# Kernel optimization log

Hardware: AMD Instinct MI355X
Metric: run time of the kernel (lower is better)

Reference implementation:

```python
import jax, jax.numpy as jnp
import numpy as np

B, TQ, TK, D, R, H = 4, 2048, 2048, 1024, 64, 512
TAU_BASE, ASTRO_DECAY = 1.0, 0.95


def setup_inputs() -> dict:
    key = jax.random.key(0)
    ks = jax.random.split(key, 20)
    xav = lambda k, din, dout: jax.random.uniform(k, (din, dout), jnp.float32, -1.0, 1.0) * np.sqrt(6.0 / (din + dout))
    inp = {
        'q_in': jax.random.normal(ks[0], (B, TQ, D), jnp.float32),
        'k_in': jax.random.normal(ks[1], (B, TK, D), jnp.float32),
        'v_in': jax.random.normal(ks[2], (B, TK, D), jnp.float32),
        'astrocyte_state': jnp.zeros((B,), jnp.float32),
        'Wq': xav(ks[3], D, D), 'bq': jnp.zeros((D,), jnp.float32),
        'Wk': xav(ks[4], D, D), 'bk': jnp.zeros((D,), jnp.float32),
        'Wv': xav(ks[5], D, D), 'bv': jnp.zeros((D,), jnp.float32),
        'Wo': xav(ks[6], D, D), 'bo': jnp.zeros((D,), jnp.float32),
        # orthonormal role rows (R <= D): QR of a random D x R matrix, rows = Q^T
        'role_matrix': jnp.linalg.qr(jax.random.normal(ks[7], (D, R), jnp.float32))[0].T,
        'Wr1': xav(ks[8], D, H), 'br1': jnp.zeros((H,), jnp.float32),
        'Wr2': xav(ks[9], H, R),
        'astro_scale': jnp.ones((1,), jnp.float32),
    }
    return inp


def _l2norm(x, axis=-1, eps=1e-12):
    return x / jnp.clip(jnp.linalg.norm(x, axis=axis, keepdims=True), eps)


def _bind_vectors(a, b):
    # holographic (circular-convolution) binding via FFT along feature dim
    n = a.shape[-1]
    return jnp.fft.irfft(jnp.fft.rfft(a, axis=-1) * jnp.fft.rfft(b, axis=-1), n=n, axis=-1)


def _compute_surprise(Q):
    # per-token surprise: RMS-normalized L2 magnitude of projected queries -> (B, T_q)
    return jnp.linalg.norm(Q, axis=-1) / np.sqrt(Q.shape[-1])


def reference(q_in, k_in, v_in, astrocyte_state, Wq, bq, Wk, bk, Wv, bv, Wo, bo,
              role_matrix, Wr1, br1, Wr2, astro_scale):
    Q = q_in @ Wq + bq                      # (B,TQ,D)
    K = k_in @ Wk + bk                      # (B,TK,D)
    V = v_in @ Wv + bv                      # (B,TK,D)

    role_mat_norm = _l2norm(role_matrix)    # (R,D)
    role_logits = jax.nn.relu(K @ Wr1 + br1) @ Wr2          # (B,TK,R)
    role_weights = jax.nn.softmax(role_logits, axis=-1)
    role_vecs = role_weights @ role_mat_norm                 # (B,TK,D)
    K_bound = _bind_vectors(K, role_vecs)                    # (B,TK,D)

    surprise = _compute_surprise(Q)                          # (B,TQ)
    mean_surprise = surprise.mean(axis=-1)                   # (B,)
    new_state = ASTRO_DECAY * astrocyte_state + (1.0 - ASTRO_DECAY) * mean_surprise
    tau_eff = TAU_BASE * jnp.clip(1.0 + astro_scale * new_state, 0.001)[:, None, None]

    q_n = _l2norm(Q)
    k_n = _l2norm(K_bound)
    cos_sim = jnp.einsum('bqd,bkd->bqk', q_n, k_n)           # (B,TQ,TK)
    x = (cos_sim + 1.0) * 0.5
    scores = jnp.clip(1.0 - tau_eff * (1.0 - x) ** 2, 0.0)   # Epanechnikov kernel
    attn = scores / jnp.clip(scores.sum(axis=-1, keepdims=True), 1e-9)
    context = jnp.einsum('bqk,bkd->bqd', attn, V)
    output = context @ Wo + bo
    return output, new_state
```

## Files before the change

### kernel.cpp

```cpp
#include <hip/hip_runtime.h>
#include <stdint.h>


#define Bq 4
#define Tq 2048
#define Dd 1024
#define NT 8192
#define Hh 512
#define Rr_ 64
#define FQ 1024

typedef unsigned short ushort_t;
typedef short s16x8 __attribute__((ext_vector_type(8)));
typedef float floatx4 __attribute__((ext_vector_type(4)));

__device__ __forceinline__ float b2f(ushort_t s) {
  unsigned u = (unsigned)s << 16;
  return __builtin_bit_cast(float, u);
}
__device__ __forceinline__ ushort_t f2b(float f) {
  unsigned u = __builtin_bit_cast(unsigned, f);
  unsigned r = (u + 0x7fffu + ((u >> 16) & 1u)) >> 16;
  return (ushort_t)r;
}
// ... 88 lines not shown
#pragma unroll
    for (int i = 0; i < 4; i++)
      af[i] = *(const s16x8*)&As[(wm + i * 16 + fr) * 32 + fk];
#pragma unroll
    for (int j = 0; j < 4; j++)
      bfv[j] = *(const s16x8*)&Bs[(wn + j * 16 + fr) * 32 + fk];
#pragma unroll
    for (int i = 0; i < 4; i++)
#pragma unroll
      for (int j = 0; j < 4; j++)
        acc[i][j] = __builtin_amdgcn_mfma_f32_16x16x32_bf16(af[i], bfv[j], acc[i][j], 0, 0, 0);
    __syncthreads();
  }

  const float tv = o.tau ? o.tau[bz] : 0.f;
  float*   Cp  = o.C   ? o.C   + (size_t)bz * o.sC : nullptr;
  ushort_t* Cb = o.Cbf ? o.Cbf + (size_t)bz * o.sC : nullptr;
  float bcv[4], cmv[4];
#pragma unroll
  for (int j = 0; j < 4; j++) {
    const int col = tn + wn + j * 16 + (lane & 15);
    bcv[j] = o.bias_col ? o.bias_col[col] : 0.f;
    cmv[j] = o.cmul ? o.cmul[(size_t)bz * o.cmulStride + col] : 1.f;
  }
#pragma unroll
  for (int i = 0; i < 4; i++) {
#pragma unroll
    for (int r = 0; r < 4; r++) {
      const int row = tm + wm + i * 16 + (lane >> 4) * 4 + r;
      const float rm = o.rmul ? o.rmul[(size_t)bz * o.rmulStride + row] : 1.f;
      const float br = o.bias_row ? o.bias_row[row] : 0.f;
      float rsum = 0.f;
#pragma unroll
      for (int j = 0; j < 4; j++) {
        const int col = tn + wn + j * 16 + (lane & 15);
        float v;
        if (o.flags & 2) {
          v = acc[i][j][r] * (rm * cmv[j]) + bcv[j] + br;
        } else {
          v = (acc[i][j][r] + bcv[j] + br) * (rm * cmv[j]);
        }
        if (o.flags & 1) v = fmaxf(v, 0.f);
        if (o.tau) { float d = 1.0f - v; v = fmaxf(1.0f - tv * 0.25f * d * d, 0.f); }
        rsum += (o.rsMode == 2) ? v * v : v;
        if (Cp) Cp[(size_t)row * o.ldc + col] = v;
        if (Cb) Cb[(size_t)row * o.ldc + col] = f2b(v);
      }
      if (o.rsMode == 1 || o.rsMode == 2) {
        rsum += __shfl_xor(rsum, 1);
        rsum += __shfl_xor(rsum, 2);
        rsum += __shfl_xor(rsum, 4);
        rsum += __shfl_xor(rsum, 8);
        if ((lane & 15) == 0)
// ... 123 lines not shown
    STAGE256(t2, 1, sl);
    __builtin_amdgcn_s_barrier();
    __builtin_amdgcn_s_setprio(1);
#pragma unroll
    for (int m = 0; m < 8; m++)
#pragma unroll
      for (int n = 2; n < 4; n++)
        acc[m][n] = __builtin_amdgcn_mfma_f32_16x16x32_bf16(a[m], b[n], acc[m][n], 0, 0, 0);
    __builtin_amdgcn_s_setprio(0);
    asm volatile("s_waitcnt vmcnt(4)" ::: "memory");
    __builtin_amdgcn_s_barrier();
  }
#undef STAGE256

  const float tv = o.tau ? o.tau[bz] : 0.f;
  float*   Cp  = o.C   ? o.C   + (size_t)bz * o.sC : nullptr;
  ushort_t* Cb = o.Cbf ? o.Cbf + (size_t)bz * o.sC : nullptr;
  float bcv[4], cmv[4];
#pragma unroll
  for (int n = 0; n < 4; n++) {
    const int col = tn + wn * 64 + n * 16 + (lane & 15);
    bcv[n] = o.bias_col ? o.bias_col[col] : 0.f;
    cmv[n] = o.cmul ? o.cmul[(size_t)bz * o.cmulStride + col] : 1.f;
  }
#pragma unroll
  for (int m = 0; m < 8; m++) {
#pragma unroll
    for (int r = 0; r < 4; r++) {
      const int row = tm + wm * 128 + m * 16 + (lane >> 4) * 4 + r;
      const float rm = o.rmul ? o.rmul[(size_t)bz * o.rmulStride + row] : 1.f;
      const float br = o.bias_row ? o.bias_row[row] : 0.f;
      float rsum = 0.f;
#pragma unroll
      for (int n = 0; n < 4; n++) {
        const int col = tn + wn * 64 + n * 16 + (lane & 15);
        float v;
        if (o.flags & 2) {
          v = acc[m][n][r] * (rm * cmv[n]) + bcv[n] + br;
        } else {
          v = (acc[m][n][r] + bcv[n] + br) * (rm * cmv[n]);
        }
        if (o.flags & 1) v = fmaxf(v, 0.f);
        if (o.tau) { float d = 1.0f - v; v = fmaxf(1.0f - tv * 0.25f * d * d, 0.f); }
        rsum += (o.rsMode == 2) ? v * v : v;
        if (Cp) Cp[(size_t)row * o.ldc + col] = v;
        if (Cb) Cb[(size_t)row * o.ldc + col] = f2b(v);
      }
      if (o.rsMode == 1 || o.rsMode == 2) {
        rsum += __shfl_xor(rsum, 1);
        rsum += __shfl_xor(rsum, 2);
        rsum += __shfl_xor(rsum, 4);
        rsum += __shfl_xor(rsum, 8);
        if ((lane & 15) == 0)
// ... 54 lines not shown
#pragma unroll
    for (int i = 0; i < 4; i++)
      af[i] = *(const s16x8*)&As[(wm + i * 16 + fr) * 32 + fk];
#pragma unroll
    for (int j = 0; j < 4; j++)
      bfv[j] = *(const s16x8*)&Bs[(wn + j * 16 + fr) * 32 + fk];
#pragma unroll
    for (int i = 0; i < 4; i++)
#pragma unroll
      for (int j = 0; j < 4; j++)
        acc[i][j] = __builtin_amdgcn_mfma_f32_16x16x32_bf16(af[i], bfv[j], acc[i][j], 0, 0, 0);
    __syncthreads();
  }

  const float tv = tau ? tau[bz] : 0.f;
  float*   Cp  = C   ? C   + (size_t)bz * sC : nullptr;
  ushort_t* Cb = Cbf ? Cbf + (size_t)bz * sC : nullptr;
  float bcv[4], cmv[4];
#pragma unroll
  for (int j = 0; j < 4; j++) {
    const int col = tn + wn + j * 16 + (lane & 15);
    bcv[j] = bias_col ? bias_col[col] : 0.f;
    cmv[j] = cmul ? cmul[(size_t)bz * cmulStride + col] : 1.f;
  }
#pragma unroll
  for (int i = 0; i < 4; i++) {
#pragma unroll
    for (int r = 0; r < 4; r++) {
      const int row = tm + wm + i * 16 + (lane >> 4) * 4 + r;
      const float rm = rmul ? rmul[(size_t)bz * rmulStride + row] : 1.f;
      const float br = bias_row ? bias_row[row] : 0.f;
      float rsum = 0.f;
#pragma unroll
      for (int j = 0; j < 4; j++) {
        const int col = tn + wn + j * 16 + (lane & 15);
        float v;
        if (flags & 2) {
          v = acc[i][j][r] * (rm * cmv[j]) + bcv[j] + br;
        } else {
          v = (acc[i][j][r] + bcv[j] + br) * (rm * cmv[j]);
        }
        if (flags & 1) v = fmaxf(v, 0.f);
        if (tau) { float d = 1.0f - v; v = fmaxf(1.0f - tv * 0.25f * d * d, 0.f); }
        rsum += (rsMode == 2) ? v * v : v;
        if (Cp) Cp[(size_t)row * ldc + col] = v;
        if (Cb) Cb[(size_t)row * ldc + col] = f2b(v);
      }
      if (rsMode == 1 || rsMode == 2) {
        rsum += __shfl_xor(rsum, 1);
        rsum += __shfl_xor(rsum, 2);
        rsum += __shfl_xor(rsum, 4);
        rsum += __shfl_xor(rsum, 8);
        if ((lane & 15) == 0)
          atomicAdd(&rowsum[(size_t)bz * rsStride + row], rsum);
      }
    }
  }
}

struct P3 { const ushort_t* A[3]; const ushort_t* Bt[3]; ushort_t* C[3]; int M[3]; };

__global__ __launch_bounds__(256) void prep3(P3 p) {
  __shared__ __align__(16) ushort_t As[128 * 32];
  __shared__ __align__(16) ushort_t Bs[128 * 32];
  const int z  = blockIdx.z;
  const int tm = blockIdx.y * 128;
  if (tm >= p.M[z]) return;
  const ushort_t* Ab = p.A[z];
  const ushort_t* Bb = p.Bt[z];
  ushort_t*       Cc = p.C[z];
  const int tn   = blockIdx.x * 128;
  const int tid  = threadIdx.x;
  const int wave = tid >> 6;
  const int lane = tid & 63;
  const int wm   = (wave & 1) << 6;
  const int wn   = (wave >> 1) << 6;
  const int sr   = lane >> 2;
  const int cp   = lane & 3;
  const int sc   = (((cp - (sr >> 1)) & 3) << 3);
  const int fr   = lane & 15;
  const int fk   = ((((lane >> 4) + (fr >> 1)) & 3) << 3);

  floatx4 acc[4][4] = {};

  for (int k0 = 0; k0 < Dd; k0 += 32) {
    {
      const ushort_t* gA0 = Ab + (size_t)(tm + wave * 16 + sr) * Dd + (k0 + sc);
      const ushort_t* gA1 = gA0 + (size_t)64 * Dd;
      char* lA = (char*)As + wave * 1024;
      load_lds16(gA0, lA);
      load_lds16(gA1, lA + 4096);
      const ushort_t* gB0 = Bb + (size_t)(tn + wave * 16 + sr) * Dd + (k0 + sc);
      const ushort_t* gB1 = gB0 + (size_t)64 * Dd;
      char* lB = (char*)Bs + wave * 1024;
      load_lds16(gB0, lB);
      load_lds16(gB1, lB + 4096);
    }
    __syncthreads();
    s16x8 af[4], bfv[4];
#pragma unroll
    for (int i = 0; i < 4; i++)
      af[i] = *(const s16x8*)&As[(wm + i * 16 + fr) * 32 + fk];
#pragma unroll
    for (int j = 0; j < 4; j++)
      bfv[j] = *(const s16x8*)&Bs[(wn + j * 16 + fr) * 32 + fk];
#pragma unroll
    for (int i = 0; i < 4; i++)
#pragma unroll
      for (int j = 0; j < 4; j++)
        acc[i][j] = __builtin_amdgcn_mfma_f32_16x16x32_bf16(af[i], bfv[j], acc[i][j], 0, 0, 0);
    __syncthreads();
  }

#pragma unroll
  for (int i = 0; i < 4; i++)
#pragma unroll
    for (int r = 0; r < 4; r++) {
      const int row = tm + wm + i * 16 + (lane >> 4) * 4 + r;
#pragma unroll
      for (int j = 0; j < 4; j++) {
        const int col = tn + wn + j * 16 + (lane & 15);
        Cc[(size_t)row * Dd + col] = f2b(acc[i][j][r]);
      }
    }
}

__global__ __launch_bounds__(256) void castbf(const float* __restrict__ in,
                                              ushort_t* __restrict__ out, int n4) {
  int i = blockIdx.x * 256 + threadIdx.x;
  if (i >= n4) return;
  float4 v = ((const float4*)in)[i];
  ushort4 o;
  o.x = f2b(v.x); o.y = f2b(v.y); o.z = f2b(v.z); o.w = f2b(v.w);
  ((ushort4*)out)[i] = o;
}

struct C3 { const float* in[3]; ushort_t* out[3]; };
__global__ __launch_bounds__(256) void castbf3(C3 p) {
  int z = blockIdx.y;
  int i = blockIdx.x * 256 + threadIdx.x;
  float4 v = ((const float4*)p.in[z])[i];
  ushort4 o;
  o.x = f2b(v.x); o.y = f2b(v.y); o.z = f2b(v.z); o.w = f2b(v.w);
  ((ushort4*)p.out[z])[i] = o;
}

struct TC4 { const float* in[4]; ushort_t* out[4]; };
__global__ __launch_bounds__(256) void tcast4(TC4 p) {
  __shared__ float t[32][33];
  int z = blockIdx.z;
  const float* in = p.in[z];
  ushort_t* out = p.out[z];
  int r0 = blockIdx.x * 32, c0 = blockIdx.y * 32;
  int x = threadIdx.x, y = threadIdx.y;
  for (int dy = 0; dy < 32; dy += 8)
    t[y + dy][x] = in[(size_t)(r0 + y + dy) * 1024 + c0 + x];
  __syncthreads();
  for (int dy = 0; dy < 32; dy += 8)
    out[(size_t)(c0 + y + dy) * 1024 + r0 + x] = f2b(t[x][y + dy]);
}

__global__ __launch_bounds__(256) void tcast(const float* __restrict__ in,
                                             ushort_t* __restrict__ out,
                                             int RrN, int Cc, int Cp) {
  __shared__ float t[32][33];
  int r0 = blockIdx.x * 32, c0 = blockIdx.y * 32;
  int x = threadIdx.x, y = threadIdx.y;
  for (int dy = 0; dy < 32; dy += 8) {
    int r = r0 + y + dy, c = c0 + x;
    t[y + dy][x] = (c < Cc) ? in[(size_t)r * Cc + c] : 0.f;
  }
  __syncthreads();
  for (int dy = 0; dy < 32; dy += 8) {
    int c = c0 + y + dy, r = r0 + x;
    if (c < Cp) out[(size_t)c * RrN + r] = f2b(t[x][y + dy]);
  }
}

__global__ __launch_bounds__(256) void rolenorm(const float* __restrict__ rm,
                                                ushort_t* __restrict__ rmn) {
  int r = blockIdx.x, tid = threadIdx.x;
  float4 v = ((const float4*)(rm + (size_t)r * 1024))[tid];
  float s = v.x * v.x + v.y * v.y + v.z * v.z + v.w * v.w;
#pragma unroll
  for (int m = 1; m < 64; m <<= 1) s += __shfl_xor(s, m);
  __shared__ float red[6];
  if ((tid & 63) == 0) red[tid >> 6] = s;
  __syncthreads();
  if (tid == 0) red[4] = 1.f / fmaxf(sqrtf(red[0] + red[1] + red[2] + red[3]), 1e-12f);
  __syncthreads();
  float inv = red[4];
  ushort4 o;
  o.x = f2b(v.x * inv); o.y = f2b(v.y * inv); o.z = f2b(v.z * inv); o.w = f2b(v.w * inv);
  ((ushort4*)(rmn + (size_t)r * 1024))[tid] = o;
}

__global__ __launch_bounds__(256) void rfn_kernel(const ushort_t* __restrict__ rmn,
                                                  const ushort_t* __restrict__ ftab,
                                                  ushort_t* __restrict__ RFnT) {
  int f = blockIdx.x;
  int t = threadIdx.x;
  int r = t >> 2, part = t & 3;
  const ushort_t* fr = ftab + (size_t)f * 1024 + part * 256;
  const ushort_t* rr = rmn + (size_t)r * 1024 + part * 256;
  float s = 0.f;
#pragma unroll 4
  for (int i = 0; i < 32; i++) {
    s16x8 a = *(const s16x8*)(fr + i * 8);
    s16x8 b = *(const s16x8*)(rr + i * 8);
#pragma unroll
    for (int j = 0; j < 8; j++) s += b2f((ushort_t)a[j]) * b2f((ushort_t)b[j]);
  }
  s += __shfl_xor(s, 1);
  s += __shfl_xor(s, 2);
  if (part == 0) RFnT[(size_t)f * 128 + r] = f2b(s);
}

__global__ __launch_bounds__(64) void foldbk(const ushort_t* __restrict__ ftab,
                                             const float* __restrict__ bk,
                                             float* __restrict__ bkF) {
  int j = blockIdx.x, lane = threadIdx.x;
  const ushort_t* row = ftab + (size_t)j * 1024 + lane * 16;
  const float* bp = bk + lane * 16;
  float s = 0.f;
#pragma unroll
  for (int i = 0; i < 2; i++) {
    s16x8 a = *(const s16x8*)(row + i * 8);
#pragma unroll
    for (int e = 0; e < 8; e++) s += b2f((ushort_t)a[e]) * bp[i * 8 + e];
  }
#pragma unroll
  for (int m = 1; m < 64; m <<= 1) s += __shfl_xor(s, m);
  if (lane == 0) bkF[j] = s;
}

__global__ __launch_bounds__(256) void foldbh(const float* __restrict__ Wr1,
                                              const float* __restrict__ bk,
                                              const float* __restrict__ br1,
                                              float* __restrict__ bh) {
  int h = blockIdx.x * 256 + threadIdx.x;
  float s = br1[h];
  for (int d = 0; d < 1024; d++) s += bk[d] * Wr1[(size_t)d * Hh + h];
  bh[h] = s;
}

__global__ __launch_bounds__(256) void foldbvo(const float* __restrict__ Wo,
                                               const float* __restrict__ bv,
                                               const float* __restrict__ bo,
                                               float* __restrict__ bvo) {
  int d = blockIdx.x * 256 + threadIdx.x;
  float s = bo[d];
  for (int e = 0; e < 1024; e++) s += bv[e] * Wo[(size_t)e * 1024 + d];
  bvo[d] = s;
}

__global__ __launch_bounds__(256) void invnorm_surprise(const float* __restrict__ ssq,
                                                        float* __restrict__ invn,
                                                        float* __restrict__ ssum) {
  int row = blockIdx.x * 256 + threadIdx.x;
  float nrm = sqrtf(ssq[row]);
  invn[row] = 1.f / fmaxf(nrm, 1e-12f);
  float t = nrm;
#pragma unroll
  for (int m = 1; m < 64; m <<= 1) t += __shfl_xor(t, m);
  if ((threadIdx.x & 63) == 0) atomicAdd(&ssum[row >> 11], t);
}

__global__ __launch_bounds__(256) void invnorm(const float* __restrict__ ssq,
                                               float* __restrict__ invn) {
  int row = blockIdx.x * 256 + threadIdx.x;
  invn[row] = 1.f / fmaxf(sqrtf(ssq[row]), 1e-12f);
}

__global__ __launch_bounds__(256) void invrowsum(const float* __restrict__ rs,
                                                 float* __restrict__ inv) {
  int row = blockIdx.x * 256 + threadIdx.x;
  inv[row] = 1.f / fmaxf(rs[row], 1e-9f);
}

__global__ void finalize_astro(const float* __restrict__ ssum, const float* __restrict__ astro,
                               const float* __restrict__ ascale, float* __restrict__ tau,
                               float* __restrict__ outTail) {
  int b = threadIdx.x;
  if (b < Bq) {
    float mean = ssum[b] * (1.f / (32.f * 2048.f));
    float ns = 0.95f * astro[b] + 0.05f * mean;
    tau[b] = fmaxf(1.f + ascale[0] * ns, 0.001f);
    outTail[b] = ns;
  }
}

__global__ __launch_bounds__(256) void softmax64(const float* __restrict__ logits,
                                                 ushort_t* __restrict__ out) {
  int row = blockIdx.x * 4 + (threadIdx.x >> 6);
  int lane = threadIdx.x & 63;
  float x = logits[(size_t)row * 128 + lane];
  float m = x;
#pragma unroll
  for (int s = 1; s < 64; s <<= 1) m = fmaxf(m, __shfl_xor(m, s));
  float e = expf(x - m);
  float sum = e;
#pragma unroll
  for (int s = 1; s < 64; s <<= 1) sum += __shfl_xor(sum, s);
  out[(size_t)row * 64 + lane] = f2b(e / sum);
}

__global__ __launch_bounds__(256) void gen_ftab(ushort_t* __restrict__ ftab) {
  const float TW = 6.283185307179586f / 1024.f;
  int idx = blockIdx.x * 256 + threadIdx.x;
  int j = idx >> 10, k = idx & 1023;
  int f = j <= 512 ? j : j - 512;
  float th = (float)((f * k) & 1023) * TW;
  float sv, cv; sincosf(th, &sv, &cv);
  ftab[idx] = f2b(j <= 512 ? cv : -sv);
}

__global__ __launch_bounds__(256) void titab(const ushort_t* __restrict__ ftab,
                                             ushort_t* __restrict__ itab) {
  __shared__ float t[32][33];
  int j0 = blockIdx.x * 32, n0 = blockIdx.y * 32;
  int x = threadIdx.x, y = threadIdx.y;
  for (int dy = 0; dy < 32; dy += 8) {
    int j = j0 + y + dy;
    float s = (j == 0 || j == 512) ? (1.f / 1024.f) : (2.f / 1024.f);
    t[y + dy][x] = b2f(ftab[(size_t)j * 1024 + n0 + x]) * s;
  }
  __syncthreads();
  for (int dy = 0; dy < 32; dy += 8)
    itab[(size_t)(n0 + y + dy) * 1024 + j0 + x] = f2b(t[x][y + dy]);
}

__global__ __launch_bounds__(256) void fftmul(const ushort_t* __restrict__ KF,
                                              const ushort_t* __restrict__ RF,
                                              ushort_t* __restrict__ P) {
  int idx = blockIdx.x * 256 + threadIdx.x;
  int t = idx >> 9;
  int j = idx & 511;
  size_t base = (size_t)t * FQ;
  if (j == 0) {
    P[base]       = f2b(b2f(KF[base]) * b2f(RF[base]));
    P[base + 512] = f2b(b2f(KF[base + 512]) * b2f(RF[base + 512]));
  } else {
    float a = b2f(KF[base + j]), b = b2f(KF[base + 512 + j]);
    float c = b2f(RF[base + j]), d = b2f(RF[base + 512 + j]);
    P[base + j]       = f2b(a * c - b * d);
    P[base + 512 + j] = f2b(a * d + b * c);
  }
}

static constexpr size_t OFF_RS    = 0;
static constexpr size_t OFF_SSQQ  = 32768;
static constexpr size_t OFF_SSQK  = 65536;
// ... 73 lines not shown
  const float* q_in  = (const float*)d_in[0];
  const float* k_in  = (const float*)d_in[1];
  const float* v_in  = (const float*)d_in[2];
  const float* astro = (const float*)d_in[3];
  const float* Wq    = (const float*)d_in[4];
  const float* bq    = (const float*)d_in[5];
  const float* Wk    = (const float*)d_in[6];
  const float* bk    = (const float*)d_in[7];
  const float* Wv    = (const float*)d_in[8];
  const float* bv    = (const float*)d_in[9];
  const float* Wo    = (const float*)d_in[10];
  const float* bo    = (const float*)d_in[11];
  const float* roleM = (const float*)d_in[12];
  const float* Wr1   = (const float*)d_in[13];
  const float* br1   = (const float*)d_in[14];
  const float* Wr2   = (const float*)d_in[15];
  const float* ascl  = (const float*)d_in[16];

  char* ws = (char*)d_ws;
  float*    rowsumS = (float*)(ws + OFF_RS);
  float*    ssqQ    = (float*)(ws + OFF_SSQQ);
  float*    ssqK    = (float*)(ws + OFF_SSQK);
  float*    invQ    = (float*)(ws + OFF_INVQ);
  float*    invK    = (float*)(ws + OFF_INVK);
  float*    invRS   = (float*)(ws + OFF_INVRS);
  float*    ssum    = (float*)(ws + OFF_SSUM);
  float*    tau     = (float*)(ws + OFF_TAU);
  ushort_t* WqT  = (ushort_t*)(ws + OFF_WQT);
  ushort_t* Wkb  = (ushort_t*)(ws + OFF_WKB);
  ushort_t* Wvb  = (ushort_t*)(ws + OFF_WVB);
  ushort_t* WoT  = (ushort_t*)(ws + OFF_WOT);
  ushort_t* Wr1T = (ushort_t*)(ws + OFF_WR1T);
  ushort_t* Wr2T = (ushort_t*)(ws + OFF_WR2T);
  ushort_t* rmn  = (ushort_t*)(ws + OFF_RMN);
  ushort_t* FTab = (ushort_t*)(ws + OFF_FTAB);
  ushort_t* ITab = (ushort_t*)(ws + OFF_ITAB);
  ushort_t* RFnT = (ushort_t*)(ws + OFF_RFNT);
  ushort_t* qbf  = (ushort_t*)(ws + OFF_B1);
  ushort_t* kbraw= (ushort_t*)(ws + OFF_B1);
  ushort_t* kinb = (ushort_t*)(ws + OFF_B2);
  ushort_t* RF   = (ushort_t*)(ws + OFF_B2);
  ushort_t* vinb = (ushort_t*)(ws + OFF_B3);
  ushort_t* Pb   = (ushort_t*)(ws + OFF_B3);
  ushort_t* qraw = (ushort_t*)(ws + OFF_B4);
  ushort_t* KF   = (ushort_t*)(ws + OFF_B5);
  ushort_t* WkF  = (ushort_t*)(ws + OFF_WKF);
  ushort_t* Wov  = (ushort_t*)(ws + OFF_WOV);
  ushort_t* WkR1 = (ushort_t*)(ws + OFF_WKR1);
  float*    bkF  = (float*)(ws + OFF_BKF);
  float*    bh   = (float*)(ws + OFF_BH);
  float*    bvo  = (float*)(ws + OFF_BVO);
  ushort_t* vT   = (ushort_t*)(ws + OFF_B7);
  ushort_t* hid  = (ushort_t*)(ws + OFF_HID);
  float*    logi = (float*)(ws + OFF_LOGI);
  ushort_t* rw   = (ushort_t*)(ws + OFF_RW);
  ushort_t* Sb   = (ushort_t*)(ws + OFF_SB);
  float*    out  = (float*)d_out;

  hipMemsetAsync(ws, 0, OFF_SSUM + 256, stream);

  TC4 tc4;
  tc4.in[0] = Wq; tc4.out[0] = WqT;
  tc4.in[1] = Wo; tc4.out[1] = WoT;
  tc4.in[2] = Wq; tc4.out[2] = WqT;
  tc4.in[3] = Wq; tc4.out[3] = WqT;
  tcast4<<<dim3(32, 32, 2), dim3(32, 8), 0, stream>>>(tc4);
  castbf<<<1024, 256, 0, stream>>>(Wk, Wkb, 262144);
  castbf<<<1024, 256, 0, stream>>>(Wv, Wvb, 262144);
  tcast<<<dim3(32, 16), dim3(32, 8), 0, stream>>>(Wr1, Wr1T, 1024, 512, 512);
  tcast<<<dim3(16, 4),  dim3(32, 8), 0, stream>>>(Wr2, Wr2T, 512, 64, 128);
  rolenorm<<<64, 256, 0, stream>>>(roleM, rmn);
  gen_ftab<<<(FQ * 1024) / 256, 256, 0, stream>>>(FTab);
  titab<<<dim3(32, 32), dim3(32, 8), 0, stream>>>(FTab, ITab);
  rfn_kernel<<<FQ, 256, 0, stream>>>(rmn, FTab, RFnT);

  P3 p3;
  p3.A[0] = FTab; p3.Bt[0] = Wkb; p3.C[0] = WkF;  p3.M[0] = 1024;
  p3.A[1] = WoT;  p3.Bt[1] = Wvb; p3.C[1] = Wov;  p3.M[1] = 1024;
  p3.A[2] = Wr1T; p3.Bt[2] = Wkb; p3.C[2] = WkR1; p3.M[2] = 512;
  prep3<<<dim3(8, 8, 3), 256, 0, stream>>>(p3);
  foldbk<<<1024, 64, 0, stream>>>(FTab, bk, bkF);
  foldbh<<<Hh / 256, 256, 0, stream>>>(Wr1, bk, br1, bh);
  foldbvo<<<Dd / 256, 256, 0, stream>>>(Wo, bv, bo, bvo);

  C3 c3;
  c3.in[0] = q_in; c3.out[0] = qbf;
  c3.in[1] = k_in; c3.out[1] = kinb;
  c3.in[2] = v_in; c3.out[2] = vinb;
  castbf3<<<dim3(8192, 3), 256, 0, stream>>>(c3);

  {
    GB gb;
    gb.op[0] = mkop(qbf, WqT, nullptr, qraw, bq, nullptr, 0, nullptr, 0, nullptr,
                    ssqQ, 0, 2, NT, Dd, Dd, Dd, Dd, Dd, 0, 0, 0, 0, 0, 128);
    gb.op[1] = mkop(kinb, WkF, nullptr, KF, bkF, nullptr, 0, nullptr, 0, nullptr,
                    nullptr, 0, 0, NT, FQ, Dd, Dd, Dd, FQ, 0, 0, 0, 0, 512, 128);
    gb.op[2] = mkop(Wov, vinb, nullptr, vT, nullptr, nullptr, 0, nullptr, 0, nullptr,
                    nullptr, 0, 0, Dd, NT, Dd, Dd, Dd, NT, 0, 0, 0, 0, 1024, 128);
    gb.op[3] = mkop(kinb, WkR1, nullptr, hid, bh, nullptr, 0, nullptr, 0, nullptr,
                    nullptr, 0, 0, NT, Hh, Dd, Dd, Dd, Hh, 0, 0, 0, 1 , 1536, 128);
    gb.nOps = 4; gb.totBlk = 1792;
    gemm_btm<<<dim3(1792), dim3(256), 0, stream>>>(gb);
  }
  invnorm_surprise<<<NT / 256, 256, 0, stream>>>(ssqQ, invQ, ssum);
  finalize_astro<<<1, 64, 0, stream>>>(ssum, astro, ascl, tau, out + (size_t)NT * Dd);

  launch_gemm(stream, hid, Wr2T, logi, nullptr, nullptr, nullptr,
              nullptr, 0, nullptr, 0, nullptr, nullptr, 0, 0,
              NT, 128, Hh, Hh, Hh, 128, 0, 0, 0, 1, 0);
  softmax64<<<NT / 4, 256, 0, stream>>>(logi, rw);
  launch_gemm(stream, rw, RFnT, nullptr, RF, nullptr, nullptr,
              nullptr, 0, nullptr, 0, nullptr, nullptr, 0, 0,
              NT, FQ, Rr_, Rr_, 128, FQ, 0, 0, 0, 1, 0);

  fftmul<<<(NT * 512) / 256, 256, 0, stream>>>(KF, RF, Pb);
  launch_gemm(stream, Pb, ITab, nullptr, kbraw, nullptr, nullptr,
              nullptr, 0, nullptr, 0, nullptr, ssqK, 0, 2,
              NT, Dd, FQ, FQ, FQ, Dd, 0, 0, 0, 1, 0);
  invnorm<<<NT / 256, 256, 0, stream>>>(ssqK, invK);

  {
    GB gb;
    GOp o = mkop(qraw, kbraw, nullptr, Sb, nullptr, invQ, Tq, invK, Tq, tau,
                 rowsumS, Tq, 1, Tq, Tq, Dd, Dd, Dd, Tq,
                 (long long)Tq * Dd, (long long)Tq * Dd, (long long)Tq * Tq, 0, 0, 256);
    gb.op[0] = o; gb.op[1] = o; gb.op[2] = o; gb.op[3] = o;
    gb.nOps = 1; gb.totBlk = 256;
    gemm256m<<<dim3(256), dim3(512), 0, stream>>>(gb);
  }
  invrowsum<<<NT / 256, 256, 0, stream>>>(rowsumS, invRS);

  launch_gemm(stream, Sb, vT, out, nullptr, bvo, nullptr,
              invRS, Tq, nullptr, 0, nullptr, nullptr, 0, 0,
              Tq, Dd, Tq, Tq, NT, Dd,
              (long long)Tq * Tq, (long long)Tq, (long long)Tq * Dd, Bq, 2 );
}
```

Measured before the change: 696.4 us.

## Merge prep kernels into two launches and fold small elementwise kernels into GEMM epilogues

Merges the many weight-preparation kernels (transposes, casts, FFT table generation, role normalization, bias folding, prep GEMMs) into two multi-role kernels, prep1 and prep2, dispatched by block index. The bias folds become partial sums combined with atomics, which requires an extra memset. The inverse-norm and inverse-rowsum kernels are removed, and their work moves into the GEMM epilogues behind new flag bits. The small Wr2 GEMM and the softmax are fused into one per-row kernel. The aim is to cut launch count and intermediate round-trips, at the cost of extra atomics and a serial dot-product path in the fused MLP kernel.

```diff
diff --git a/kernel.cpp b/kernel.cpp
--- a/kernel.cpp
+++ b/kernel.cpp
@@ -134,13 +134,15 @@
     const int col = tn + wn + j * 16 + (lane & 15);
     bcv[j] = o.bias_col ? o.bias_col[col] : 0.f;
     cmv[j] = o.cmul ? o.cmul[(size_t)bz * o.cmulStride + col] : 1.f;
+    if (o.flags & 4) cmv[j] = 1.f / fmaxf(sqrtf(cmv[j]), 1e-12f);
   }
 #pragma unroll
   for (int i = 0; i < 4; i++) {
 #pragma unroll
     for (int r = 0; r < 4; r++) {
       const int row = tm + wm + i * 16 + (lane >> 4) * 4 + r;
-      const float rm = o.rmul ? o.rmul[(size_t)bz * o.rmulStride + row] : 1.f;
+      float rm = o.rmul ? o.rmul[(size_t)bz * o.rmulStride + row] : 1.f;
+      if (o.flags & 8) rm = 1.f / fmaxf(rm, 1e-9f);
       const float br = o.bias_row ? o.bias_row[row] : 0.f;
       float rsum = 0.f;
 #pragma unroll
@@ -310,13 +312,15 @@
     const int col = tn + wn * 64 + n * 16 + (lane & 15);
     bcv[n] = o.bias_col ? o.bias_col[col] : 0.f;
     cmv[n] = o.cmul ? o.cmul[(size_t)bz * o.cmulStride + col] : 1.f;
+    if (o.flags & 4) cmv[n] = 1.f / fmaxf(sqrtf(cmv[n]), 1e-12f);
   }
 #pragma unroll
   for (int m = 0; m < 8; m++) {
 #pragma unroll
     for (int r = 0; r < 4; r++) {
       const int row = tm + wm * 128 + m * 16 + (lane >> 4) * 4 + r;
-      const float rm = o.rmul ? o.rmul[(size_t)bz * o.rmulStride + row] : 1.f;
+      float rm = o.rmul ? o.rmul[(size_t)bz * o.rmulStride + row] : 1.f;
+      if (o.flags & 8) rm = 1.f / fmaxf(rm, 1e-9f);
       const float br = o.bias_row ? o.bias_row[row] : 0.f;
       float rsum = 0.f;
 #pragma unroll
@@ -417,13 +421,15 @@
     const int col = tn + wn + j * 16 + (lane & 15);
     bcv[j] = bias_col ? bias_col[col] : 0.f;
     cmv[j] = cmul ? cmul[(size_t)bz * cmulStride + col] : 1.f;
+    if (flags & 4) cmv[j] = 1.f / fmaxf(sqrtf(cmv[j]), 1e-12f);
   }
 #pragma unroll
   for (int i = 0; i < 4; i++) {
 #pragma unroll
     for (int r = 0; r < 4; r++) {
       const int row = tm + wm + i * 16 + (lane >> 4) * 4 + r;
-      const float rm = rmul ? rmul[(size_t)bz * rmulStride + row] : 1.f;
+      float rm = rmul ? rmul[(size_t)bz * rmulStride + row] : 1.f;
+      if (flags & 8) rm = 1.f / fmaxf(rm, 1e-9f);
       const float br = bias_row ? bias_row[row] : 0.f;
       float rsum = 0.f;
 #pragma unroll
@@ -453,200 +459,276 @@
   }
 }
 
-struct P3 { const ushort_t* A[3]; const ushort_t* Bt[3]; ushort_t* C[3]; int M[3]; };
-
-__global__ __launch_bounds__(256) void prep3(P3 p) {
+struct P1args {
+  const float *Wq, *Wo, *Wk, *Wv, *Wr1, *Wr2, *roleM, *q_in, *k_in, *v_in;
+  ushort_t *WqT, *WoT, *Wkb, *Wvb, *Wr1T, *Wr2T, *rmn, *FTab, *qbf, *kinb, *vinb;
+};
+
+__global__ __launch_bounds__(256) void prep1(P1args p) {
+  __shared__ float t[32][33];
+  __shared__ float red[6];
+  int b = blockIdx.x;
+  const int tid = threadIdx.x;
+
+  if (b < 4096) {
+    const float TW = 6.283185307179586f / 1024.f;
+    int idx = b * 256 + tid;
+    int j = idx >> 10, k = idx & 1023;
+    int f = j <= 512 ? j : j - 512;
+    float th = (float)((f * k) & 1023) * TW;
+    float sv, cv; sincosf(th, &sv, &cv);
+    p.FTab[idx] = f2b(j <= 512 ? cv : -sv);
+    return;
+  }
+  b -= 4096;
+  if (b < 2048) {
+    const float* in = b < 1024 ? p.Wq : p.Wo;
+    ushort_t* out   = b < 1024 ? p.WqT : p.WoT;
+    int bb = b & 1023;
+    int r0 = (bb & 31) * 32, c0 = (bb >> 5) * 32;
+    int x = tid & 31, y = tid >> 5;
+    for (int dy = 0; dy < 32; dy += 8)
+      t[y + dy][x] = in[(size_t)(r0 + y + dy) * 1024 + c0 + x];
+    __syncthreads();
+    for (int dy = 0; dy < 32; dy += 8)
+      out[(size_t)(c0 + y + dy) * 1024 + r0 + x] = f2b(t[x][y + dy]);
+    return;
+  }
+  b -= 2048;
+  if (b < 2048) {
+    const float* in = b < 1024 ? p.Wk : p.Wv;
+    ushort_t* out   = b < 1024 ? p.Wkb : p.Wvb;
+    int i = (b & 1023) * 256 + tid;
+    float4 v = ((const float4*)in)[i];
+    ushort4 o;
+    o.x = f2b(v.x); o.y = f2b(v.y); o.z = f2b(v.z); o.w = f2b(v.w);
+    ((ushort4*)out)[i] = o;
+    return;
+  }
+  b -= 2048;
+  if (b < 512) {
+    int r0 = (b & 31) * 32, c0 = (b >> 5) * 32;
+    int x = tid & 31, y = tid >> 5;
+    for (int dy = 0; dy < 32; dy += 8)
+      t[y + dy][x] = p.Wr1[(size_t)(r0 + y + dy) * 512 + c0 + x];
+    __syncthreads();
+    for (int dy = 0; dy < 32; dy += 8)
+      p.Wr1T[(size_t)(c0 + y + dy) * 1024 + r0 + x] = f2b(t[x][y + dy]);
+    return;
+  }
+  b -= 512;
+  if (b < 64) {
+    int r0 = (b & 15) * 32, c0 = (b >> 4) * 32;
+    int x = tid & 31, y = tid >> 5;
+    for (int dy = 0; dy < 32; dy += 8) {
+      int r = r0 + y + dy, c = c0 + x;
+      t[y + dy][x] = (c < 64) ? p.Wr2[(size_t)r * 64 + c] : 0.f;
+    }
+    __syncthreads();
+    for (int dy = 0; dy < 32; dy += 8)
+      p.Wr2T[(size_t)(c0 + y + dy) * 512 + r0 + x] = f2b(t[x][y + dy]);
+    return;
+  }
+  b -= 64;
+  if (b < 64) {
+    int r = b;
+    float4 v = ((const float4*)(p.roleM + (size_t)r * 1024))[tid];
+    float s = v.x * v.x + v.y * v.y + v.z * v.z + v.w * v.w;
+#pragma unroll
+    for (int m = 1; m < 64; m <<= 1) s += __shfl_xor(s, m);
+    if ((tid & 63) == 0) red[tid >> 6] = s;
+    __syncthreads();
+    if (tid == 0) red[4] = 1.f / fmaxf(sqrtf(red[0] + red[1] + red[2] + red[3]), 1e-12f);
+    __syncthreads();
+    float inv = red[4];
+    ushort4 o;
+    o.x = f2b(v.x * inv); o.y = f2b(v.y * inv); o.z = f2b(v.z * inv); o.w = f2b(v.w * inv);
+    ((ushort4*)(p.rmn + (size_t)r * 1024))[tid] = o;
+    return;
+  }
+  b -= 64;
+  {
+    const float* in; ushort_t* out;
+    if (b < 8192)      { in = p.q_in; out = p.qbf; }
+    else if (b < 16384){ in = p.k_in; out = p.kinb; b -= 8192; }
+    else               { in = p.v_in; out = p.vinb; b -= 16384; }
+    int i = b * 256 + tid;
+    float4 v = ((const float4*)in)[i];
+    ushort4 o;
+    o.x = f2b(v.x); o.y = f2b(v.y); o.z = f2b(v.z); o.w = f2b(v.w);
+    ((ushort4*)out)[i] = o;
+  }
+}
+
+struct P2args {
+  const ushort_t *FTab, *rmn, *Wkb, *Wvb, *WoT, *Wr1T;
+  const float *bk, *br1, *bv, *bo, *Wr1, *Wo;
+  ushort_t *ITab, *RFnT, *WkF, *Wov, *WkR1;
+  float *bkF, *bh, *bvo;
+};
+
+__global__ __launch_bounds__(256) void prep2(P2args p) {
   __shared__ __align__(16) ushort_t As[128 * 32];
   __shared__ __align__(16) ushort_t Bs[128 * 32];
-  const int z  = blockIdx.z;
-  const int tm = blockIdx.y * 128;
-  if (tm >= p.M[z]) return;
-  const ushort_t* Ab = p.A[z];
-  const ushort_t* Bb = p.Bt[z];
-  ushort_t*       Cc = p.C[z];
-  const int tn   = blockIdx.x * 128;
-  const int tid  = threadIdx.x;
-  const int wave = tid >> 6;
-  const int lane = tid & 63;
-  const int wm   = (wave & 1) << 6;
-  const int wn   = (wave >> 1) << 6;
-  const int sr   = lane >> 2;
-  const int cp   = lane & 3;
-  const int sc   = (((cp - (sr >> 1)) & 3) << 3);
-  const int fr   = lane & 15;
-  const int fk   = ((((lane >> 4) + (fr >> 1)) & 3) << 3);
-
-  floatx4 acc[4][4] = {};
-
-  for (int k0 = 0; k0 < Dd; k0 += 32) {
-    {
-      const ushort_t* gA0 = Ab + (size_t)(tm + wave * 16 + sr) * Dd + (k0 + sc);
-      const ushort_t* gA1 = gA0 + (size_t)64 * Dd;
-      char* lA = (char*)As + wave * 1024;
-      load_lds16(gA0, lA);
-      load_lds16(gA1, lA + 4096);
-      const ushort_t* gB0 = Bb + (size_t)(tn + wave * 16 + sr) * Dd + (k0 + sc);
-      const ushort_t* gB1 = gB0 + (size_t)64 * Dd;
-      char* lB = (char*)Bs + wave * 1024;
-      load_lds16(gB0, lB);
-      load_lds16(gB1, lB + 4096);
+  __shared__ float t[32][33];
+  int b = blockIdx.x;
+  const int tid = threadIdx.x;
+
+  if (b < 1024) {
+    int j0 = (b & 31) * 32, n0 = (b >> 5) * 32;
+    int x = tid & 31, y = tid >> 5;
+    for (int dy = 0; dy < 32; dy += 8) {
+      int j = j0 + y + dy;
+      float s = (j == 0 || j == 512) ? (1.f / 1024.f) : (2.f / 1024.f);
+      t[y + dy][x] = b2f(p.FTab[(size_t)j * 1024 + n0 + x]) * s;
     }
     __syncthreads();
-    s16x8 af[4], bfv[4];
+    for (int dy = 0; dy < 32; dy += 8)
+      p.ITab[(size_t)(n0 + y + dy) * 1024 + j0 + x] = f2b(t[x][y + dy]);
+    return;
+  }
+  b -= 1024;
+  if (b < 1024) {
+    int f = b;
+    int r = tid >> 2, part = tid & 3;
+    const ushort_t* fr = p.FTab + (size_t)f * 1024 + part * 256;
+    const ushort_t* rr = p.rmn + (size_t)r * 1024 + part * 256;
+    float s = 0.f;
+#pragma unroll 4
+    for (int i = 0; i < 32; i++) {
+      s16x8 a = *(const s16x8*)(fr + i * 8);
+      s16x8 bb = *(const s16x8*)(rr + i * 8);
+#pragma unroll
+      for (int j = 0; j < 8; j++) s += b2f((ushort_t)a[j]) * b2f((ushort_t)bb[j]);
+    }
+    s += __shfl_xor(s, 1);
+    s += __shfl_xor(s, 2);
+    if (part == 0) p.RFnT[(size_t)f * 128 + r] = f2b(s);
+    return;
+  }
+  b -= 1024;
+  if (b < 256) {
+    int j = b * 4 + (tid >> 6);
+    int lane = tid & 63;
+    const ushort_t* row = p.FTab + (size_t)j * 1024 + lane * 16;
+    const float* bp = p.bk + lane * 16;
+    float s = 0.f;
+#pragma unroll
+    for (int i = 0; i < 2; i++) {
+      s16x8 a = *(const s16x8*)(row + i * 8);
+#pragma unroll
+      for (int e = 0; e < 8; e++) s += b2f((ushort_t)a[e]) * bp[i * 8 + e];
+    }
+#pragma unroll
+    for (int m = 1; m < 64; m <<= 1) s += __shfl_xor(s, m);
+    if (lane == 0) p.bkF[j] = s;
+    return;
+  }
+  b -= 256;
+  if (b < 32) {
+    int h = (b & 1) * 256 + tid;
+    int d0 = (b >> 1) * 64;
+    float s = ((b >> 1) == 0) ? p.br1[h] : 0.f;
+    for (int i = 0; i < 64; i++)
+      s += p.bk[d0 + i] * p.Wr1[(size_t)(d0 + i) * Hh + h];
+    atomicAdd(&p.bh[h], s);
+    return;
+  }
+  b -= 32;
+  if (b < 64) {
+    int d = (b & 3) * 256 + tid;
+    int e0 = (b >> 2) * 64;
+    float s = ((b >> 2) == 0) ? p.bo[d] : 0.f;
+    for (int i = 0; i < 64; i++)
+      s += p.bv[e0 + i] * p.Wo[(size_t)(e0 + i) * 1024 + d];
+    atomicAdd(&p.bvo[d], s);
+    return;
+  }
+  b -= 64;
+  {
+    const int z = b >> 6;
+    const int rem = b & 63;
+    const int by = rem >> 3, bx = rem & 7;
+    if (z == 2 && by >= 4) return;
+    const ushort_t* Ab = (z == 0) ? p.FTab : (z == 1) ? p.WoT : p.Wr1T;
+    const ushort_t* Bb = (z == 1) ? p.Wvb : p.Wkb;
+    ushort_t* Cc = (z == 0) ? p.WkF : (z == 1) ? p.Wov : p.WkR1;
+    const int tm = by * 128, tn = bx * 128;
+    const int wave = tid >> 6, lane = tid & 63;
+    const int wm = (wave & 1) << 6, wn = (wave >> 1) << 6;
+    const int sr = lane >> 2, cp = lane & 3;
+    const int sc = (((cp - (sr >> 1)) & 3) << 3);
+    const int fr = lane & 15;
+    const int fk = ((((lane >> 4) + (fr >> 1)) & 3) << 3);
+
+    floatx4 acc[4][4] = {};
+    for (int k0 = 0; k0 < Dd; k0 += 32) {
+      {
+        const ushort_t* gA0 = Ab + (size_t)(tm + wave * 16 + sr) * Dd + (k0 + sc);
+        const ushort_t* gA1 = gA0 + (size_t)64 * Dd;
+        char* lA = (char*)As + wave * 1024;
+        load_lds16(gA0, lA);
+        load_lds16(gA1, lA + 4096);
+        const ushort_t* gB0 = Bb + (size_t)(tn + wave * 16 + sr) * Dd + (k0 + sc);
+        const ushort_t* gB1 = gB0 + (size_t)64 * Dd;
+        char* lB = (char*)Bs + wave * 1024;
+        load_lds16(gB0, lB);
+        load_lds16(gB1, lB + 4096);
+      }
+      __syncthreads();
+      s16x8 af[4], bfv[4];
+#pragma unroll
+      for (int i = 0; i < 4; i++)
+        af[i] = *(const s16x8*)&As[(wm + i * 16 + fr) * 32 + fk];
+#pragma unroll
+      for (int j = 0; j < 4; j++)
+        bfv[j] = *(const s16x8*)&Bs[(wn + j * 16 + fr) * 32 + fk];
+#pragma unroll
+      for (int i = 0; i < 4; i++)
+#pragma unroll
+        for (int j = 0; j < 4; j++)
+          acc[i][j] = __builtin_amdgcn_mfma_f32_16x16x32_bf16(af[i], bfv[j], acc[i][j], 0, 0, 0);
+      __syncthreads();
+    }
 #pragma unroll
     for (int i = 0; i < 4; i++)
-      af[i] = *(const s16x8*)&As[(wm + i * 16 + fr) * 32 + fk];
-#pragma unroll
-    for (int j = 0; j < 4; j++)
-      bfv[j] = *(const s16x8*)&Bs[(wn + j * 16 + fr) * 32 + fk];
-#pragma unroll
-    for (int i = 0; i < 4; i++)
-#pragma unroll
-      for (int j = 0; j < 4; j++)
-        acc[i][j] = __builtin_amdgcn_mfma_f32_16x16x32_bf16(af[i], bfv[j], acc[i][j], 0, 0, 0);
-    __syncthreads();
-  }
-
-#pragma unroll
-  for (int i = 0; i < 4; i++)
-#pragma unroll
-    for (int r = 0; r < 4; r++) {
-      const int row = tm + wm + i * 16 + (lane >> 4) * 4 + r;
-#pragma unroll
-      for (int j = 0; j < 4; j++) {
-        const int col = tn + wn + j * 16 + (lane & 15);
-        Cc[(size_t)row * Dd + col] = f2b(acc[i][j][r]);
+#pragma unroll
+      for (int r = 0; r < 4; r++) {
+        const int row = tm + wm + i * 16 + (lane >> 4) * 4 + r;
+#pragma unroll
+        for (int j = 0; j < 4; j++) {
+          const int col = tn + wn + j * 16 + (lane & 15);
+          Cc[(size_t)row * Dd + col] = f2b(acc[i][j][r]);
+        }
       }
-    }
-}
-
-__global__ __launch_bounds__(256) void castbf(const float* __restrict__ in,
-                                              ushort_t* __restrict__ out, int n4) {
-  int i = blockIdx.x * 256 + threadIdx.x;
-  if (i >= n4) return;
-  float4 v = ((const float4*)in)[i];
-  ushort4 o;
-  o.x = f2b(v.x); o.y = f2b(v.y); o.z = f2b(v.z); o.w = f2b(v.w);
-  ((ushort4*)out)[i] = o;
-}
-
-struct C3 { const float* in[3]; ushort_t* out[3]; };
-__global__ __launch_bounds__(256) void castbf3(C3 p) {
-  int z = blockIdx.y;
-  int i = blockIdx.x * 256 + threadIdx.x;
-  float4 v = ((const float4*)p.in[z])[i];
-  ushort4 o;
-  o.x = f2b(v.x); o.y = f2b(v.y); o.z = f2b(v.z); o.w = f2b(v.w);
-  ((ushort4*)p.out[z])[i] = o;
-}
-
-struct TC4 { const float* in[4]; ushort_t* out[4]; };
-__global__ __launch_bounds__(256) void tcast4(TC4 p) {
-  __shared__ float t[32][33];
-  int z = blockIdx.z;
-  const float* in = p.in[z];
-  ushort_t* out = p.out[z];
-  int r0 = blockIdx.x * 32, c0 = blockIdx.y * 32;
-  int x = threadIdx.x, y = threadIdx.y;
-  for (int dy = 0; dy < 32; dy += 8)
-    t[y + dy][x] = in[(size_t)(r0 + y + dy) * 1024 + c0 + x];
+  }
+}
+
+__global__ __launch_bounds__(256) void mlp2sm(const ushort_t* __restrict__ hid,
+                                              const ushort_t* __restrict__ Wr2T,
+                                              ushort_t* __restrict__ rw) {
+  __shared__ __align__(16) ushort_t hrow[4][512];
+  const int w = threadIdx.x >> 6, lane = threadIdx.x & 63;
+  const int row = blockIdx.x * 4 + w;
+  *(s16x8*)&hrow[w][lane * 8] = *(const s16x8*)&hid[(size_t)row * 512 + lane * 8];
   __syncthreads();
-  for (int dy = 0; dy < 32; dy += 8)
-    out[(size_t)(c0 + y + dy) * 1024 + r0 + x] = f2b(t[x][y + dy]);
-}
-
-__global__ __launch_bounds__(256) void tcast(const float* __restrict__ in,
-                                             ushort_t* __restrict__ out,
-                                             int RrN, int Cc, int Cp) {
-  __shared__ float t[32][33];
-  int r0 = blockIdx.x * 32, c0 = blockIdx.y * 32;
-  int x = threadIdx.x, y = threadIdx.y;
-  for (int dy = 0; dy < 32; dy += 8) {
-    int r = r0 + y + dy, c = c0 + x;
-    t[y + dy][x] = (c < Cc) ? in[(size_t)r * Cc + c] : 0.f;
-  }
-  __syncthreads();
-  for (int dy = 0; dy < 32; dy += 8) {
-    int c = c0 + y + dy, r = r0 + x;
-    if (c < Cp) out[(size_t)c * RrN + r] = f2b(t[x][y + dy]);
-  }
-}
-
-__global__ __launch_bounds__(256) void rolenorm(const float* __restrict__ rm,
-                                                ushort_t* __restrict__ rmn) {
-  int r = blockIdx.x, tid = threadIdx.x;
-  float4 v = ((const float4*)(rm + (size_t)r * 1024))[tid];
-  float s = v.x * v.x + v.y * v.y + v.z * v.z + v.w * v.w;
-#pragma unroll
-  for (int m = 1; m < 64; m <<= 1) s += __shfl_xor(s, m);
-  __shared__ float red[6];
-  if ((tid & 63) == 0) red[tid >> 6] = s;
-  __syncthreads();
-  if (tid == 0) red[4] = 1.f / fmaxf(sqrtf(red[0] + red[1] + red[2] + red[3]), 1e-12f);
-  __syncthreads();
-  float inv = red[4];
-  ushort4 o;
-  o.x = f2b(v.x * inv); o.y = f2b(v.y * inv); o.z = f2b(v.z * inv); o.w = f2b(v.w * inv);
-  ((ushort4*)(rmn + (size_t)r * 1024))[tid] = o;
-}
-
-__global__ __launch_bounds__(256) void rfn_kernel(const ushort_t* __restrict__ rmn,
-                                                  const ushort_t* __restrict__ ftab,
-                                                  ushort_t* __restrict__ RFnT) {
-  int f = blockIdx.x;
-  int t = threadIdx.x;
-  int r = t >> 2, part = t & 3;
-  const ushort_t* fr = ftab + (size_t)f * 1024 + part * 256;
-  const ushort_t* rr = rmn + (size_t)r * 1024 + part * 256;
+  const ushort_t* wrow = Wr2T + (size_t)lane * 512;
   float s = 0.f;
-#pragma unroll 4
-  for (int i = 0; i < 32; i++) {
-    s16x8 a = *(const s16x8*)(fr + i * 8);
-    s16x8 b = *(const s16x8*)(rr + i * 8);
-#pragma unroll
-    for (int j = 0; j < 8; j++) s += b2f((ushort_t)a[j]) * b2f((ushort_t)b[j]);
-  }
-  s += __shfl_xor(s, 1);
-  s += __shfl_xor(s, 2);
-  if (part == 0) RFnT[(size_t)f * 128 + r] = f2b(s);
-}
-
-__global__ __launch_bounds__(64) void foldbk(const ushort_t* __restrict__ ftab,
-                                             const float* __restrict__ bk,
-                                             float* __restrict__ bkF) {
-  int j = blockIdx.x, lane = threadIdx.x;
-  const ushort_t* row = ftab + (size_t)j * 1024 + lane * 16;
-  const float* bp = bk + lane * 16;
-  float s = 0.f;
-#pragma unroll
-  for (int i = 0; i < 2; i++) {
-    s16x8 a = *(const s16x8*)(row + i * 8);
-#pragma unroll
-    for (int e = 0; e < 8; e++) s += b2f((ushort_t)a[e]) * bp[i * 8 + e];
-  }
-#pragma unroll
-  for (int m = 1; m < 64; m <<= 1) s += __shfl_xor(s, m);
-  if (lane == 0) bkF[j] = s;
-}
-
-__global__ __launch_bounds__(256) void foldbh(const float* __restrict__ Wr1,
-                                              const float* __restrict__ bk,
-                                              const float* __restrict__ br1,
-                                              float* __restrict__ bh) {
-  int h = blockIdx.x * 256 + threadIdx.x;
-  float s = br1[h];
-  for (int d = 0; d < 1024; d++) s += bk[d] * Wr1[(size_t)d * Hh + h];
-  bh[h] = s;
-}
-
-__global__ __launch_bounds__(256) void foldbvo(const float* __restrict__ Wo,
-                                               const float* __restrict__ bv,
-                                               const float* __restrict__ bo,
-                                               float* __restrict__ bvo) {
-  int d = blockIdx.x * 256 + threadIdx.x;
-  float s = bo[d];
-  for (int e = 0; e < 1024; e++) s += bv[e] * Wo[(size_t)e * 1024 + d];
-  bvo[d] = s;
+#pragma unroll 8
+  for (int i = 0; i < 64; i++) {
+    s16x8 a = *(const s16x8*)&hrow[w][i * 8];
+    s16x8 bb = *(const s16x8*)&wrow[i * 8];
+#pragma unroll
+    for (int j = 0; j < 8; j++) s += b2f((ushort_t)a[j]) * b2f((ushort_t)bb[j]);
+  }
+  float m = s;
+#pragma unroll
+  for (int d = 1; d < 64; d <<= 1) m = fmaxf(m, __shfl_xor(m, d));
+  float e = expf(s - m);
+  float sum = e;
+#pragma unroll
+  for (int d = 1; d < 64; d <<= 1) sum += __shfl_xor(sum, d);
+  rw[(size_t)row * 64 + lane] = f2b(e / sum);
 }
 
 __global__ __launch_bounds__(256) void invnorm_surprise(const float* __restrict__ ssq,
@@ -659,18 +741,6 @@
 #pragma unroll
   for (int m = 1; m < 64; m <<= 1) t += __shfl_xor(t, m);
   if ((threadIdx.x & 63) == 0) atomicAdd(&ssum[row >> 11], t);
-}
-
-__global__ __launch_bounds__(256) void invnorm(const float* __restrict__ ssq,
-                                               float* __restrict__ invn) {
-  int row = blockIdx.x * 256 + threadIdx.x;
-  invn[row] = 1.f / fmaxf(sqrtf(ssq[row]), 1e-12f);
-}
-
-__global__ __launch_bounds__(256) void invrowsum(const float* __restrict__ rs,
-                                                 float* __restrict__ inv) {
-  int row = blockIdx.x * 256 + threadIdx.x;
-  inv[row] = 1.f / fmaxf(rs[row], 1e-9f);
 }
 
 __global__ void finalize_astro(const float* __restrict__ ssum, const float* __restrict__ astro,
@@ -683,46 +753,6 @@
     tau[b] = fmaxf(1.f + ascale[0] * ns, 0.001f);
     outTail[b] = ns;
   }
-}
-
-__global__ __launch_bounds__(256) void softmax64(const float* __restrict__ logits,
-                                                 ushort_t* __restrict__ out) {
-  int row = blockIdx.x * 4 + (threadIdx.x >> 6);
-  int lane = threadIdx.x & 63;
-  float x = logits[(size_t)row * 128 + lane];
-  float m = x;
-#pragma unroll
-  for (int s = 1; s < 64; s <<= 1) m = fmaxf(m, __shfl_xor(m, s));
-  float e = expf(x - m);
-  float sum = e;
-#pragma unroll
-  for (int s = 1; s < 64; s <<= 1) sum += __shfl_xor(sum, s);
-  out[(size_t)row * 64 + lane] = f2b(e / sum);
-}
-
-__global__ __launch_bounds__(256) void gen_ftab(ushort_t* __restrict__ ftab) {
-  const float TW = 6.283185307179586f / 1024.f;
-  int idx = blockIdx.x * 256 + threadIdx.x;
-  int j = idx >> 10, k = idx & 1023;
-  int f = j <= 512 ? j : j - 512;
-  float th = (float)((f * k) & 1023) * TW;
-  float sv, cv; sincosf(th, &sv, &cv);
-  ftab[idx] = f2b(j <= 512 ? cv : -sv);
-}
-
-__global__ __launch_bounds__(256) void titab(const ushort_t* __restrict__ ftab,
-                                             ushort_t* __restrict__ itab) {
-  __shared__ float t[32][33];
-  int j0 = blockIdx.x * 32, n0 = blockIdx.y * 32;
-  int x = threadIdx.x, y = threadIdx.y;
-  for (int dy = 0; dy < 32; dy += 8) {
-    int j = j0 + y + dy;
-    float s = (j == 0 || j == 512) ? (1.f / 1024.f) : (2.f / 1024.f);
-    t[y + dy][x] = b2f(ftab[(size_t)j * 1024 + n0 + x]) * s;
-  }
-  __syncthreads();
-  for (int dy = 0; dy < 32; dy += 8)
-    itab[(size_t)(n0 + y + dy) * 1024 + j0 + x] = f2b(t[x][y + dy]);
 }
 
 __global__ __launch_bounds__(256) void fftmul(const ushort_t* __restrict__ KF,
@@ -842,8 +872,6 @@
   float*    ssqQ    = (float*)(ws + OFF_SSQQ);
   float*    ssqK    = (float*)(ws + OFF_SSQK);
   float*    invQ    = (float*)(ws + OFF_INVQ);
-  float*    invK    = (float*)(ws + OFF_INVK);
-  float*    invRS   = (float*)(ws + OFF_INVRS);
   float*    ssum    = (float*)(ws + OFF_SSUM);
   float*    tau     = (float*)(ws + OFF_TAU);
   ushort_t* WqT  = (ushort_t*)(ws + OFF_WQT);
@@ -872,42 +900,28 @@
   float*    bvo  = (float*)(ws + OFF_BVO);
   ushort_t* vT   = (ushort_t*)(ws + OFF_B7);
   ushort_t* hid  = (ushort_t*)(ws + OFF_HID);
-  float*    logi = (float*)(ws + OFF_LOGI);
   ushort_t* rw   = (ushort_t*)(ws + OFF_RW);
   ushort_t* Sb   = (ushort_t*)(ws + OFF_SB);
   float*    out  = (float*)d_out;
 
   hipMemsetAsync(ws, 0, OFF_SSUM + 256, stream);
-
-  TC4 tc4;
-  tc4.in[0] = Wq; tc4.out[0] = WqT;
-  tc4.in[1] = Wo; tc4.out[1] = WoT;
-  tc4.in[2] = Wq; tc4.out[2] = WqT;
-  tc4.in[3] = Wq; tc4.out[3] = WqT;
-  tcast4<<<dim3(32, 32, 2), dim3(32, 8), 0, stream>>>(tc4);
-  castbf<<<1024, 256, 0, stream>>>(Wk, Wkb, 262144);
-  castbf<<<1024, 256, 0, stream>>>(Wv, Wvb, 262144);
-  tcast<<<dim3(32, 16), dim3(32, 8), 0, stream>>>(Wr1, Wr1T, 1024, 512, 512);
-  tcast<<<dim3(16, 4),  dim3(32, 8), 0, stream>>>(Wr2, Wr2T, 512, 64, 128);
-  rolenorm<<<64, 256, 0, stream>>>(roleM, rmn);
-  gen_ftab<<<(FQ * 1024) / 256, 256, 0, stream>>>(FTab);
-  titab<<<dim3(32, 32), dim3(32, 8), 0, stream>>>(FTab, ITab);
-  rfn_kernel<<<FQ, 256, 0, stream>>>(rmn, FTab, RFnT);
-
-  P3 p3;
-  p3.A[0] = FTab; p3.Bt[0] = Wkb; p3.C[0] = WkF;  p3.M[0] = 1024;
-  p3.A[1] = WoT;  p3.Bt[1] = Wvb; p3.C[1] = Wov;  p3.M[1] = 1024;
-  p3.A[2] = Wr1T; p3.Bt[2] = Wkb; p3.C[2] = WkR1; p3.M[2] = 512;
-  prep3<<<dim3(8, 8, 3), 256, 0, stream>>>(p3);
-  foldbk<<<1024, 64, 0, stream>>>(FTab, bk, bkF);
-  foldbh<<<Hh / 256, 256, 0, stream>>>(Wr1, bk, br1, bh);
-  foldbvo<<<Dd / 256, 256, 0, stream>>>(Wo, bv, bo, bvo);
-
-  C3 c3;
-  c3.in[0] = q_in; c3.out[0] = qbf;
-  c3.in[1] = k_in; c3.out[1] = kinb;
-  c3.in[2] = v_in; c3.out[2] = vinb;
-  castbf3<<<dim3(8192, 3), 256, 0, stream>>>(c3);
+  hipMemsetAsync(ws + OFF_BH, 0, (OFF_BVO - OFF_BH) + 4096, stream);
+
+  P1args p1;
+  p1.Wq = Wq; p1.Wo = Wo; p1.Wk = Wk; p1.Wv = Wv; p1.Wr1 = Wr1; p1.Wr2 = Wr2;
+  p1.roleM = roleM; p1.q_in = q_in; p1.k_in = k_in; p1.v_in = v_in;
+  p1.WqT = WqT; p1.WoT = WoT; p1.Wkb = Wkb; p1.Wvb = Wvb; p1.Wr1T = Wr1T;
+  p1.Wr2T = Wr2T; p1.rmn = rmn; p1.FTab = FTab;
+  p1.qbf = qbf; p1.kinb = kinb; p1.vinb = vinb;
+  prep1<<<dim3(33408), dim3(256), 0, stream>>>(p1);
+
+  P2args p2;
+  p2.FTab = FTab; p2.rmn = rmn; p2.Wkb = Wkb; p2.Wvb = Wvb; p2.WoT = WoT;
+  p2.Wr1T = Wr1T; p2.bk = bk; p2.br1 = br1; p2.bv = bv; p2.bo = bo;
+  p2.Wr1 = Wr1; p2.Wo = Wo;
+  p2.ITab = ITab; p2.RFnT = RFnT; p2.WkF = WkF; p2.Wov = Wov; p2.WkR1 = WkR1;
+  p2.bkF = bkF; p2.bh = bh; p2.bvo = bvo;
+  prep2<<<dim3(2592), dim3(256), 0, stream>>>(p2);
 
   {
     GB gb;
@@ -925,10 +939,8 @@
   invnorm_surprise<<<NT / 256, 256, 0, stream>>>(ssqQ, invQ, ssum);
   finalize_astro<<<1, 64, 0, stream>>>(ssum, astro, ascl, tau, out + (size_t)NT * Dd);
 
-  launch_gemm(stream, hid, Wr2T, logi, nullptr, nullptr, nullptr,
-              nullptr, 0, nullptr, 0, nullptr, nullptr, 0, 0,
-              NT, 128, Hh, Hh, Hh, 128, 0, 0, 0, 1, 0);
-  softmax64<<<NT / 4, 256, 0, stream>>>(logi, rw);
+  mlp2sm<<<dim3(NT / 4), dim3(256), 0, stream>>>(hid, Wr2T, rw);
+
   launch_gemm(stream, rw, RFnT, nullptr, RF, nullptr, nullptr,
               nullptr, 0, nullptr, 0, nullptr, nullptr, 0, 0,
               NT, FQ, Rr_, Rr_, 128, FQ, 0, 0, 0, 1, 0);
@@ -937,21 +949,21 @@
   launch_gemm(stream, Pb, ITab, nullptr, kbraw, nullptr, nullptr,
               nullptr, 0, nullptr, 0, nullptr, ssqK, 0, 2,
               NT, Dd, FQ, FQ, FQ, Dd, 0, 0, 0, 1, 0);
-  invnorm<<<NT / 256, 256, 0, stream>>>(ssqK, invK);
 
   {
     GB gb;
-    GOp o = mkop(qraw, kbraw, nullptr, Sb, nullptr, invQ, Tq, invK, Tq, tau,
+    GOp o = mkop(qraw, kbraw, nullptr, Sb, nullptr, invQ, Tq, ssqK, Tq, tau,
                  rowsumS, Tq, 1, Tq, Tq, Dd, Dd, Dd, Tq,
-                 (long long)Tq * Dd, (long long)Tq * Dd, (long long)Tq * Tq, 0, 0, 256);
+                 (long long)Tq * Dd, (long long)Tq * Dd, (long long)Tq * Tq,
+                 4 , 0, 256);
     gb.op[0] = o; gb.op[1] = o; gb.op[2] = o; gb.op[3] = o;
     gb.nOps = 1; gb.totBlk = 256;
     gemm256m<<<dim3(256), dim3(512), 0, stream>>>(gb);
   }
-  invrowsum<<<NT / 256, 256, 0, stream>>>(rowsumS, invRS);
 
   launch_gemm(stream, Sb, vT, out, nullptr, bvo, nullptr,
-              invRS, Tq, nullptr, 0, nullptr, nullptr, 0, 0,
+              rowsumS, Tq, nullptr, 0, nullptr, nullptr, 0, 0,
               Tq, Dd, Tq, Tq, NT, Dd,
-              (long long)Tq * Tq, (long long)Tq, (long long)Tq * Dd, Bq, 2 );
-}
+              (long long)Tq * Tq, (long long)Tq, (long long)Tq * Dd, Bq,
+              2 | 8 );
+}
```

Result: faster. 637.5 us (-8.5%).
